# Optimization experiments

Measured on AMD Instinct MI355X. Metric: run time of the kernel, lower is better.

Reference implementation:

```python
import jax, jax.numpy as jnp
import numpy as np

BS, H = 2048, 1024
XDIM = 2048 + 4 * 64  # x + R*W = 2304
IN = XDIM + 2 * H     # 4352


def setup_inputs() -> dict:
    key = jax.random.key(0)
    ks = jax.random.split(key, 11)
    s = 1.0 / np.sqrt(IN)  # torch Linear default init scale
    return {
        "input_x": jax.random.normal(ks[0], (BS, XDIM), jnp.float32),
        "previous_time": jax.random.normal(ks[1], (BS, H), jnp.float32),
        "previous_layer": jax.random.normal(ks[2], (BS, H), jnp.float32),
        "old_state": jnp.zeros((BS, H), jnp.float32),
        "Wi": jax.random.normal(ks[3], (H, IN), jnp.float32) * s,
        "bi": jax.random.normal(ks[4], (H,), jnp.float32) * s,
        "Wf": jax.random.normal(ks[5], (H, IN), jnp.float32) * s,
        "bf": jax.random.normal(ks[6], (H,), jnp.float32) * s,
        "Wo": jax.random.normal(ks[7], (H, IN), jnp.float32) * s,
        "bo": jax.random.normal(ks[8], (H,), jnp.float32) * s,
        "Ws": jax.random.normal(ks[9], (H, IN), jnp.float32) * s,
        "bs_state": jax.random.normal(ks[10], (H,), jnp.float32) * s,
    }


def reference(input_x, previous_time, previous_layer, old_state,
              Wi, bi, Wf, bf, Wo, bo, Ws, bs_state):
    # semicolon_input: [bs, x + R*W + 2h]
    z = jnp.concatenate([input_x, previous_time, previous_layer], axis=1)
    # Fuse the four projections into one GEMM: [bs, 4h]
    W_all = jnp.concatenate([Wi, Wf, Wo, Ws], axis=0)          # [4h, IN]
    b_all = jnp.concatenate([bi, bf, bo, bs_state], axis=0)    # [4h]
    proj = z @ W_all.T + b_all
    gi, gf, go, gs = jnp.split(proj, 4, axis=1)
    input_gate = jax.nn.sigmoid(gi)
    forget_gate = jax.nn.sigmoid(gf)
    output_gate = jax.nn.sigmoid(go)
    new_state = forget_gate * old_state + input_gate * jnp.tanh(gs)
    new_hidden = output_gate * jnp.tanh(new_state)
    return new_hidden
```

## Files before the change

### kernel.cpp

```cpp
#include <hip/hip_runtime.h>
#include <stdint.h>
#include <stddef.h>

#define M_DIM 2048
#define N_DIM 4096
#define K_DIM 4352
#define H_DIM 1024
#define X_DIM 2304

#define A_OFF 0u
#define B_OFF 17825792u

typedef __bf16 bf16x8 __attribute__((ext_vector_type(8)));
typedef float f32x4 __attribute__((ext_vector_type(4)));

__device__ __forceinline__ unsigned short f32_to_bf16(float f) {
    unsigned u = __float_as_uint(f);
    u += 0x7FFFu + ((u >> 16) & 1u);
    return (unsigned short)(u >> 16);
}

__device__ __forceinline__ float sigm_(float x) { return 1.f / (1.f + __expf(-x)); }
__device__ __forceinline__ float tanh_(float x) {
    x = fminf(15.f, fmaxf(-15.f, x));
    float e = __expf(2.f * x);
    return (e - 1.f) / (e + 1.f);
}

__global__ __launch_bounds__(256) void convert_kernel(
    const float* __restrict__ x, const float* __restrict__ pt,
    const float* __restrict__ pl,
    const float* __restrict__ Wi, const float* __restrict__ Wf,
    const float* __restrict__ Wo, const float* __restrict__ Ws,
    unsigned short* __restrict__ Abf, unsigned short* __restrict__ Bbf)
{
    const int row = blockIdx.x;
    const float* srow = nullptr;
    unsigned short* drow;
    if (row < M_DIM) {
        drow = Abf + (size_t)row * K_DIM;
    } else {
        int n = row - M_DIM;
        int g = n >> 10, h = n & 1023;
        const float* W = (g == 0) ? Wi : (g == 1) ? Wf : (g == 2) ? Wo : Ws;
        srow = W + (size_t)h * K_DIM;
        drow = Bbf + (size_t)(h * 4 + g) * K_DIM;
    }

    for (int c8 = threadIdx.x; c8 < K_DIM / 8; c8 += 256) {
        int col = c8 * 8;
        const float* s;
        if (row < M_DIM) {
            if (col < X_DIM)              s = x  + (size_t)row * X_DIM + col;
            else if (col < X_DIM + H_DIM) s = pt + (size_t)row * H_DIM + (col - X_DIM);
            else                          s = pl + (size_t)row * H_DIM + (col - X_DIM - H_DIM);
        } else {
            s = srow + col;
        }
        float4 v0 = ((const float4*)s)[0];
        float4 v1 = ((const float4*)s)[1];
        union { unsigned short h[8]; uint4 u; } r;
        r.h[0] = f32_to_bf16(v0.x); r.h[1] = f32_to_bf16(v0.y);
        r.h[2] = f32_to_bf16(v0.z); r.h[3] = f32_to_bf16(v0.w);
        r.h[4] = f32_to_bf16(v1.x); r.h[5] = f32_to_bf16(v1.y);
        r.h[6] = f32_to_bf16(v1.z); r.h[7] = f32_to_bf16(v1.w);
        *(uint4*)(drow + col) = r.u;
    }
}

__global__ __launch_bounds__(256) void gemm_fused(
    const unsigned short* __restrict__ A,
    const unsigned short* __restrict__ B,
    const float* __restrict__ old_state,
    const float* __restrict__ bi, const float* __restrict__ bfv,
    const float* __restrict__ bo, const float* __restrict__ bs,
    float* __restrict__ out)
{
    __shared__ __align__(16) char smem[65536];
    float* sP = (float*)smem;

    const int tid  = threadIdx.x;
    const int lane = tid & 63;
    const int wave = tid >> 6;
    const int wm = (wave >> 1) * 64;
    const int wn = (wave & 1) * 64;

    const int b   = blockIdx.x;
    const int xcd = b & 7;
    const int j   = b >> 3;
    const int n0  = (xcd * 4 + (j & 3)) * 128;
    const int m0  = (j >> 2) * 128;

    const int srow = wave * 8 + (lane >> 3);
    const int c8s  = ((lane & 7) ^ (lane >> 3)) * 8;

    const int fr  = lane & 15;
    const int sw  = fr & 7;
    const int kb0 = lane >> 4;

    f32x4 acc[4][4];
#pragma unroll
    for (int i = 0; i < 4; ++i)
#pragma unroll
        for (int jj = 0; jj < 4; ++jj) acc[i][jj] = (f32x4){0.f, 0.f, 0.f, 0.f};

    const unsigned short* Aw = A + (size_t)(m0 + srow) * K_DIM + c8s;
    const unsigned short* Bw = B + (size_t)(n0 + srow) * K_DIM + c8s;

    auto stage = [&](int kt, int bufOff) {
#pragma unroll
        for (int i = 0; i < 4; ++i) {
            __builtin_amdgcn_global_load_lds(
                (const __attribute__((address_space(1))) unsigned*)(Aw + (size_t)i * 32 * K_DIM + kt),
                (__attribute__((address_space(3))) unsigned*)(smem + bufOff + i * 4096 + wave * 1024),
                16, 0, 0);
            __builtin_amdgcn_global_load_lds(
                (const __attribute__((address_space(1))) unsigned*)(Bw + (size_t)i * 32 * K_DIM + kt),
                (__attribute__((address_space(3))) unsigned*)(smem + bufOff + 16384 + i * 4096 + wave * 1024),
                16, 0, 0);
        }
    };

    auto compute = [&](int bufOff) {
        const unsigned short* sA = (const unsigned short*)(smem + bufOff);
        const unsigned short* sB = (const unsigned short*)(smem + bufOff + 16384);
#pragma unroll
        for (int kk = 0; kk < 64; kk += 32) {
            const int kb = kk / 8 + kb0;
            bf16x8 af[4], bfr[4];
#pragma unroll
            for (int i = 0; i < 4; ++i) {
                const int ra  = wm + i * 16 + fr;
                const int rb_ = wn + i * 16 + fr;
                af[i]  = *(const bf16x8*)(sA + (ra  * 8 + (kb ^ sw)) * 8);
                bfr[i] = *(const bf16x8*)(sB + (rb_ * 8 + (kb ^ sw)) * 8);
            }
#pragma unroll
            for (int i = 0; i < 4; ++i)
#pragma unroll
                for (int jj = 0; jj < 4; ++jj)
                    acc[i][jj] = __builtin_amdgcn_mfma_f32_16x16x32_bf16(
                        af[i], bfr[jj], acc[i][jj], 0, 0, 0);
        }
    };

    stage(0, 0);

    for (int kt = 0; kt < K_DIM; kt += 128) {
        __syncthreads();
        if (kt + 64 < K_DIM) stage(kt + 64, 32768);
        compute(0);
        __syncthreads();
        if (kt + 128 < K_DIM) stage(kt + 128, 0);
        compute(32768);
    }

    const int cw = lane & 15;
    const int rw = (lane >> 4) * 4;
    const int hl = tid & 15;
    const int rb = tid >> 4;

    for (int p = 0; p < 2; ++p) {
        __syncthreads();
        if ((wave & 1) == p) {
#pragma unroll
            for (int i = 0; i < 4; ++i)
#pragma unroll
                for (int jj = 0; jj < 4; ++jj)
#pragma unroll
                    for (int r = 0; r < 4; ++r)
                        sP[(wm + i * 16 + rw + r) * 76 + jj * 16 + cw] = acc[i][jj][r];
        }
        __syncthreads();

        const int hg = (n0 >> 2) + p * 16 + hl;
        const float b_i = bi[hg], b_f = bfv[hg], b_o = bo[hg], b_s = bs[hg];
#pragma unroll
        for (int k = 0; k < 8; ++k) {
            const int row = rb + 16 * k;
            float4 g = *(const float4*)(sP + row * 76 + hl * 4);
            const size_t oidx = (size_t)(m0 + row) * H_DIM + hg;
            float old = old_state[oidx];
            float ig = sigm_(g.x + b_i);
            float fg = sigm_(g.y + b_f);
            float og = sigm_(g.z + b_o);
            float ts = tanh_(g.w + b_s);
            out[oidx] = og * tanh_(fg * old + ig * ts);
        }
    }
}

extern "C" void kernel_launch(void* const* d_in, const int* in_sizes, int n_in,
                              void* d_out, int out_size, void* d_ws, size_t ws_size,
                              hipStream_t stream) {
    const float* x   = (const float*)d_in[0];
    const float* pt  = (const float*)d_in[1];
    const float* pl  = (const float*)d_in[2];
    const float* old = (const float*)d_in[3];
    const float* Wi  = (const float*)d_in[4];
    const float* bi  = (const float*)d_in[5];
    const float* Wf  = (const float*)d_in[6];
    const float* bf  = (const float*)d_in[7];
    const float* Wo  = (const float*)d_in[8];
    const float* bo  = (const float*)d_in[9];
    const float* Ws  = (const float*)d_in[10];
    const float* bs  = (const float*)d_in[11];
    float* out = (float*)d_out;

    char* ws = (char*)d_ws;
    unsigned short* Abf = (unsigned short*)(ws + A_OFF);
    unsigned short* Bbf = (unsigned short*)(ws + B_OFF);

    convert_kernel<<<M_DIM + N_DIM, 256, 0, stream>>>(x, pt, pl, Wi, Wf, Wo, Ws, Abf, Bbf);

    gemm_fused<<<512, 256, 0, stream>>>(Abf, Bbf, old, bi, bf, bo, bs, out);
}
```

Before: 232.9 us.

## Use 128x256 tiles with 8 waves and a 4-stage LDS pipeline

The GEMM moves to 512-thread blocks computing 128x256 output tiles, halving the grid to 256 blocks. K steps drop to 32 and run through a four-buffer LDS ring with explicit vmcnt waits, raw s_barrier, sched_barrier and setprio around the MFMA bursts, so global-to-LDS loads stay three stages ahead. The LDS swizzle and the epilogue are reworked for the wider tile. The aim is more A reuse and better overlap of loads with MFMA work. The cost is 96KB of LDS and fewer blocks (256 on a 256-CU part, so one wave of blocks), which may limit latency hiding.

Result: no change. 231.7 us (-0.5%).

```diff
diff --git a/kernel.cpp b/kernel.cpp
--- a/kernel.cpp
+++ b/kernel.cpp
@@ -68,7 +68,7 @@
     }
 }
 
-__global__ __launch_bounds__(256) void gemm_fused(
+__global__ __launch_bounds__(512, 2) void gemm_fused(
     const unsigned short* __restrict__ A,
     const unsigned short* __restrict__ B,
     const float* __restrict__ old_state,
@@ -76,27 +76,32 @@
     const float* __restrict__ bo, const float* __restrict__ bs,
     float* __restrict__ out)
 {
-    __shared__ __align__(16) char smem[65536];
+    __shared__ __align__(16) char smem[98304];
     float* sP = (float*)smem;
 
     const int tid  = threadIdx.x;
     const int lane = tid & 63;
     const int wave = tid >> 6;
-    const int wm = (wave >> 1) * 64;
-    const int wn = (wave & 1) * 64;
+    const int wm = (wave >> 2) * 64;
+    const int wn = (wave & 3) * 64;
 
     const int b   = blockIdx.x;
     const int xcd = b & 7;
     const int j   = b >> 3;
-    const int n0  = (xcd * 4 + (j & 3)) * 128;
-    const int m0  = (j >> 2) * 128;
-
-    const int srow = wave * 8 + (lane >> 3);
-    const int c8s  = ((lane & 7) ^ (lane >> 3)) * 8;
+    const int m0  = (j >> 1) * 128;
+    const int n0  = (xcd * 2 + (j & 1)) * 256;
+
+    const int srow_ = tid >> 2;
+    const int kb_   = (tid & 3) ^ ((tid >> 3) & 3);
+    const unsigned short* Asrc  = A + (size_t)(m0 + srow_)       * K_DIM + kb_ * 8;
+    const unsigned short* Bsrc0 = B + (size_t)(n0 + srow_)       * K_DIM + kb_ * 8;
+    const unsigned short* Bsrc1 = B + (size_t)(n0 + 128 + srow_) * K_DIM + kb_ * 8;
 
     const int fr  = lane & 15;
-    const int sw  = fr & 7;
     const int kb0 = lane >> 4;
+    const int swz = (kb0 ^ ((fr >> 1) & 3)) * 16;
+    const int aoff = (wm + fr) * 64 + swz;
+    const int boff = 8192 + (wn + fr) * 64 + swz;
 
     f32x4 acc[4][4];
 #pragma unroll
@@ -104,65 +109,81 @@
 #pragma unroll
         for (int jj = 0; jj < 4; ++jj) acc[i][jj] = (f32x4){0.f, 0.f, 0.f, 0.f};
 
-    const unsigned short* Aw = A + (size_t)(m0 + srow) * K_DIM + c8s;
-    const unsigned short* Bw = B + (size_t)(n0 + srow) * K_DIM + c8s;
-
-    auto stage = [&](int kt, int bufOff) {
-#pragma unroll
-        for (int i = 0; i < 4; ++i) {
-            __builtin_amdgcn_global_load_lds(
-                (const __attribute__((address_space(1))) unsigned*)(Aw + (size_t)i * 32 * K_DIM + kt),
-                (__attribute__((address_space(3))) unsigned*)(smem + bufOff + i * 4096 + wave * 1024),
-                16, 0, 0);
-            __builtin_amdgcn_global_load_lds(
-                (const __attribute__((address_space(1))) unsigned*)(Bw + (size_t)i * 32 * K_DIM + kt),
-                (__attribute__((address_space(3))) unsigned*)(smem + bufOff + 16384 + i * 4096 + wave * 1024),
-                16, 0, 0);
-        }
+    auto stage = [&](int h, int c) {
+        const size_t koff = (size_t)h * 32;
+        __builtin_amdgcn_global_load_lds(
+            (const __attribute__((address_space(1))) unsigned*)(Asrc + koff),
+            (__attribute__((address_space(3))) unsigned*)(smem + c * 24576 + wave * 1024),
+            16, 0, 0);
+        __builtin_amdgcn_global_load_lds(
+            (const __attribute__((address_space(1))) unsigned*)(Bsrc0 + koff),
+            (__attribute__((address_space(3))) unsigned*)(smem + c * 24576 + 8192 + wave * 1024),
+            16, 0, 0);
+        __builtin_amdgcn_global_load_lds(
+            (const __attribute__((address_space(1))) unsigned*)(Bsrc1 + koff),
+            (__attribute__((address_space(3))) unsigned*)(smem + c * 24576 + 16384 + wave * 1024),
+            16, 0, 0);
     };
 
-    auto compute = [&](int bufOff) {
-        const unsigned short* sA = (const unsigned short*)(smem + bufOff);
-        const unsigned short* sB = (const unsigned short*)(smem + bufOff + 16384);
-#pragma unroll
-        for (int kk = 0; kk < 64; kk += 32) {
-            const int kb = kk / 8 + kb0;
-            bf16x8 af[4], bfr[4];
-#pragma unroll
-            for (int i = 0; i < 4; ++i) {
-                const int ra  = wm + i * 16 + fr;
-                const int rb_ = wn + i * 16 + fr;
-                af[i]  = *(const bf16x8*)(sA + (ra  * 8 + (kb ^ sw)) * 8);
-                bfr[i] = *(const bf16x8*)(sB + (rb_ * 8 + (kb ^ sw)) * 8);
-            }
-#pragma unroll
-            for (int i = 0; i < 4; ++i)
-#pragma unroll
-                for (int jj = 0; jj < 4; ++jj)
-                    acc[i][jj] = __builtin_amdgcn_mfma_f32_16x16x32_bf16(
-                        af[i], bfr[jj], acc[i][jj], 0, 0, 0);
-        }
-    };
-
-    stage(0, 0);
-
-    for (int kt = 0; kt < K_DIM; kt += 128) {
-        __syncthreads();
-        if (kt + 64 < K_DIM) stage(kt + 64, 32768);
-        compute(0);
-        __syncthreads();
-        if (kt + 128 < K_DIM) stage(kt + 128, 0);
-        compute(32768);
-    }
+#define VM6 asm volatile("s_waitcnt vmcnt(6)" ::: "memory")
+#define VM3 asm volatile("s_waitcnt vmcnt(3)" ::: "memory")
+#define VM0 asm volatile("s_waitcnt vmcnt(0)" ::: "memory")
+#define VMNONE ((void)0)
+
+#define PHASE(C, SH, DOSTAGE, VMLINE)                                           \
+    do {                                                                        \
+        bf16x8 af[4], bq[4];                                                    \
+        _Pragma("unroll")                                                       \
+        for (int i_ = 0; i_ < 4; ++i_) {                                        \
+            af[i_] = *(const bf16x8*)(smem + (C) * 24576 + aoff + i_ * 1024);   \
+            bq[i_] = *(const bf16x8*)(smem + (C) * 24576 + boff + i_ * 1024);   \
+        }                                                                       \
+        if (DOSTAGE) stage((SH), ((C) + 3) & 3);                                \
+        __builtin_amdgcn_s_barrier();                                           \
+        asm volatile("s_waitcnt lgkmcnt(0)" ::: "memory");                      \
+        __builtin_amdgcn_sched_barrier(0);                                      \
+        __builtin_amdgcn_s_setprio(1);                                          \
+        _Pragma("unroll")                                                       \
+        for (int i_ = 0; i_ < 4; ++i_)                                          \
+            _Pragma("unroll")                                                   \
+            for (int j_ = 0; j_ < 4; ++j_)                                      \
+                acc[i_][j_] = __builtin_amdgcn_mfma_f32_16x16x32_bf16(          \
+                    af[i_], bq[j_], acc[i_][j_], 0, 0, 0);                      \
+        __builtin_amdgcn_s_setprio(0);                                          \
+        __builtin_amdgcn_sched_barrier(0);                                      \
+        VMLINE;                                                                 \
+        __builtin_amdgcn_s_barrier();                                           \
+    } while (0)
+
+    stage(0, 0); stage(1, 1); stage(2, 2);
+    VM6;
+    __builtin_amdgcn_s_barrier();
+
+    for (int h4 = 0; h4 < 132; h4 += 4) {
+        PHASE(0, h4 + 3, true, VM6);
+        PHASE(1, h4 + 4, true, VM6);
+        PHASE(2, h4 + 5, true, VM6);
+        PHASE(3, h4 + 6, true, VM6);
+    }
+    PHASE(0, 135, true,  VM6);
+    PHASE(1, 0,   false, VM3);
+    PHASE(2, 0,   false, VM0);
+    PHASE(3, 0,   false, VMNONE);
+
+#undef PHASE
+#undef VM6
+#undef VM3
+#undef VM0
+#undef VMNONE
 
     const int cw = lane & 15;
     const int rw = (lane >> 4) * 4;
     const int hl = tid & 15;
     const int rb = tid >> 4;
 
-    for (int p = 0; p < 2; ++p) {
+    for (int p = 0; p < 4; ++p) {
         __syncthreads();
-        if ((wave & 1) == p) {
+        if ((wave & 3) == p) {
 #pragma unroll
             for (int i = 0; i < 4; ++i)
 #pragma unroll
@@ -176,8 +197,8 @@
         const int hg = (n0 >> 2) + p * 16 + hl;
         const float b_i = bi[hg], b_f = bfv[hg], b_o = bo[hg], b_s = bs[hg];
 #pragma unroll
-        for (int k = 0; k < 8; ++k) {
-            const int row = rb + 16 * k;
+        for (int k = 0; k < 4; ++k) {
+            const int row = rb + 32 * k;
             float4 g = *(const float4*)(sP + row * 76 + hl * 4);
             const size_t oidx = (size_t)(m0 + row) * H_DIM + hg;
             float old = old_state[oidx];
@@ -213,5 +234,5 @@
 
     convert_kernel<<<M_DIM + N_DIM, 256, 0, stream>>>(x, pt, pl, Wi, Wf, Wo, Ws, Abf, Bbf);
 
-    gemm_fused<<<512, 256, 0, stream>>>(Abf, Bbf, old, bi, bf, bo, bs, out);
-}
+    gemm_fused<<<256, 512, 0, stream>>>(Abf, Bbf, old, bi, bf, bo, bs, out);
+}
```
